# Kernel optimization log

Hardware: AMD Instinct MI355X
Metric: run time of the kernel (lower is better)

The kernel has to match this reference:

```python
import jax, jax.numpy as jnp
import numpy as np

B, SQ, SKV, DIN, DOUT = 8, 2048, 2048, 512, 512

def setup_inputs() -> dict:
    key = jax.random.key(0)
    ks = jax.random.split(key, 8)
    s = 1.0 / np.sqrt(DIN)
    return {
        "query": jax.random.normal(ks[0], (B, SQ, DIN), jnp.float32),
        "key": jax.random.normal(ks[1], (B, SKV, DIN), jnp.float32),
        "value": jax.random.normal(ks[2], (B, SKV, DIN), jnp.float32),
        "offset": jax.random.normal(ks[3], (B, SQ, DIN), jnp.float32),
        "Wq": jax.random.normal(ks[4], (DIN, DOUT), jnp.float32) * s,
        "Wk": jax.random.normal(ks[5], (DIN, DOUT), jnp.float32) * s,
        "Wv": jax.random.normal(ks[6], (DIN, DOUT), jnp.float32) * s,
        "Woff": jax.random.normal(ks[7], (DIN, SKV), jnp.float32) * s,
    }

def reference(query, key, value, offset, Wq, Wk, Wv, Woff):
    # q/k/v projections (nn.Linear, no bias)
    q = jnp.einsum("bqi,io->bqo", query, Wq)   # [B,SQ,DOUT]
    k = jnp.einsum("bki,io->bko", key, Wk)     # [B,SKV,DOUT]
    v = jnp.einsum("bki,io->bko", value, Wv)   # [B,SKV,DOUT]
    scale = 1.0 / jnp.sqrt(jnp.asarray(q.shape[-1], jnp.float32))
    scores = jnp.einsum("bqd,bkd->bqk", q, k) * scale  # [B,SQ,SKV]
    attn = jax.nn.softmax(scores, axis=-1)
    # offset bias is added AFTER softmax (no renormalization), per original
    attn = attn + jnp.einsum("bqi,ik->bqk", offset, Woff)
    return jnp.einsum("bqk,bkd->bqd", attn, v)  # [B,SQ,DOUT]
```

## Files before the change

### kernel.cpp

```cpp
#include <hip/hip_runtime.h>
#include <hip/hip_bf16.h>
#include <stdint.h>

typedef __bf16 bf16;
typedef bf16 bf16x4_t __attribute__((ext_vector_type(4)));
typedef bf16 bf16x8_t __attribute__((ext_vector_type(8)));
typedef float floatx4_t __attribute__((ext_vector_type(4)));

#define NB 8
#define SQ 2048
#define SKV 2048
#define DIN 512
#define DOUT 512

__device__ __forceinline__ void load_lds16(const bf16* g, bf16* l) {
    __builtin_amdgcn_global_load_lds(
        (const __attribute__((address_space(1))) unsigned int*)g,
        (__attribute__((address_space(3))) unsigned int*)l, 16, 0, 0);
}

struct CastArgs {
    const float* src[6];
    bf16* dst[6];
    int n4[6];
};
__global__ void cast_many(CastArgs a) {
    int z = blockIdx.z;
    int i = blockIdx.x * blockDim.x + threadIdx.x;
    if (i >= a.n4[z]) return;
    if (!a.src[z]) {
        bf16x4_t zo = { (bf16)0.f, (bf16)0.f, (bf16)0.f, (bf16)0.f };
        ((bf16x4_t*)a.dst[z])[i] = zo;
        return;
    }
    float4 f = ((const float4*)a.src[z])[i];
    bf16x4_t o = { (bf16)f.x, (bf16)f.y, (bf16)f.z, (bf16)f.w };
    ((bf16x4_t*)a.dst[z])[i] = o;
}

struct TWArgs { const float* src[3]; bf16* dst[3]; float scl[3]; };
__global__ void transpose_w(TWArgs a) {
    __shared__ float t[32][33];
    const float* src = a.src[blockIdx.z];
    bf16* dst = a.dst[blockIdx.z];
    const float s = a.scl[blockIdx.z];
    int tx = threadIdx.x, ty = threadIdx.y;
    int x0 = blockIdx.x * 32, y0 = blockIdx.y * 32;
#pragma unroll
    for (int j = 0; j < 4; ++j)
        t[ty + 8 * j][tx] = src[(y0 + ty + 8 * j) * DIN + x0 + tx];
    __syncthreads();
#pragma unroll
    for (int j = 0; j < 4; ++j)
        dst[(x0 + ty + 8 * j) * DIN + y0 + tx] = (bf16)(t[tx][ty + 8 * j] * s);
}

__device__ __forceinline__ void gemm_mainloop(
    floatx4_t (&acc)[4][4], const bf16* __restrict__ Ap, const bf16* __restrict__ Bp,
    int lda, int ldb, int K, bf16* As, bf16* Bs, int wave, int lane)
{
    const int wm = (wave & 1) * 64, wn = (wave >> 1) * 64;
    const int lm = lane & 15, quad = lane >> 4;
    const int srow = lane >> 2, scol = (lane & 3) * 8;
    for (int k0 = 0; k0 < K; k0 += 64) {
        __syncthreads();
#pragma unroll
        for (int p = 0; p < 2; ++p) {
#pragma unroll
            for (int t = 0; t < 2; ++t) {
                const int r0 = (wave * 2 + t) * 16;
                load_lds16(Ap + (long long)(r0 + srow) * lda + (k0 + p * 32 + scol),
                           &As[p * 4096 + r0 * 32]);
                load_lds16(Bp + (long long)(r0 + srow) * ldb + (k0 + p * 32 + scol),
                           &Bs[p * 4096 + r0 * 32]);
            }
        }
        __syncthreads();
#pragma unroll
        for (int p = 0; p < 2; ++p) {
            bf16x8_t af[4], bfr[4];
#pragma unroll
            for (int i = 0; i < 4; ++i)
                af[i] = *(const bf16x8_t*)&As[p * 4096 + (wm + i * 16 + lm) * 32 + quad * 8];
#pragma unroll
            for (int i = 0; i < 4; ++i)
                bfr[i] = *(const bf16x8_t*)&Bs[p * 4096 + (wn + i * 16 + lm) * 32 + quad * 8];
#pragma unroll
            for (int i = 0; i < 4; ++i)
#pragma unroll
                for (int j = 0; j < 4; ++j)
                    acc[i][j] = __builtin_amdgcn_mfma_f32_16x16x32_bf16(af[i], bfr[j], acc[i][j], 0, 0, 0);
        }
    }
}

__global__ __launch_bounds__(256) void proj_gemm(
    const bf16* __restrict__ QKin, const bf16* __restrict__ WqkT, bf16* __restrict__ QKout,
    const bf16* __restrict__ valueb, const bf16* __restrict__ WvT, bf16* __restrict__ VT)
{
    __shared__ bf16 As[2 * 128 * 32];
    __shared__ bf16 Bs[2 * 128 * 32];
    const int tid = threadIdx.x;
    const int wave = tid >> 6, lane = tid & 63;
    const int wm = (wave & 1) * 64, wn = (wave >> 1) * 64;
    const int lm = lane & 15, quad = lane >> 4;
    const int id = blockIdx.x;

    floatx4_t acc[4][4];
#pragma unroll
    for (int i = 0; i < 4; ++i)
#pragma unroll
        for (int j = 0; j < 4; ++j) acc[i][j] = 0.0f;

    if (id < 1024) {
        const int xcd = id & 7, t = id >> 3, m = t & 3;
        const int gg = xcd + 8 * (t >> 2);
        const int y = gg & 127, z = gg >> 7;
        const bf16* Ap = QKin + (long long)z * (NB * SQ * DIN) + (long long)y * 128 * DIN;
        const bf16* Bp = WqkT + (long long)z * (DIN * DOUT) + (long long)m * 128 * DIN;
        gemm_mainloop(acc, Ap, Bp, DIN, DIN, DIN, As, Bs, wave, lane);
        bf16* C = QKout + (long long)z * (NB * SQ * DOUT);
#pragma unroll
        for (int i = 0; i < 4; ++i)
#pragma unroll
            for (int j = 0; j < 4; ++j) {
                const long long row0 = (long long)y * 128 + wm + i * 16 + quad * 4;
                const int col = m * 128 + wn + j * 16 + lm;
#pragma unroll
                for (int r = 0; r < 4; ++r)
                    C[(row0 + r) * DOUT + col] = (bf16)acc[i][j][r];
            }
    } else {
        const int id2 = id - 1024;
        const int z = id2 & 7, r2 = id2 >> 3;
        const int ym = r2 & 3, xn = r2 >> 2;
        const bf16* Ap = WvT + (long long)ym * 128 * DIN;
        const bf16* Bp = valueb + (long long)z * (SKV * DIN) + (long long)xn * 128 * DIN;
        gemm_mainloop(acc, Ap, Bp, DIN, DIN, DIN, As, Bs, wave, lane);
        bf16* C = VT + (long long)z * (DOUT * SKV);
#pragma unroll
        for (int i = 0; i < 4; ++i)
#pragma unroll
            for (int j = 0; j < 4; ++j) {
                const long long row0 = (long long)ym * 128 + wm + i * 16 + quad * 4;
                const int col = xn * 128 + wn + j * 16 + lm;
#pragma unroll
                for (int r = 0; r < 4; ++r)
                    C[(row0 + r) * SKV + col] = (bf16)acc[i][j][r];
            }
    }
}

__global__ __launch_bounds__(256) void g_gemm(
    const bf16* __restrict__ VT, const bf16* __restrict__ Woffb, bf16* __restrict__ G)
{
    __shared__ bf16 As[2 * 128 * 32];
    __shared__ bf16 Bs[2 * 128 * 32];
    const int tid = threadIdx.x;
    const int wave = tid >> 6, lane = tid & 63;
    const int id = blockIdx.x;
    const int z = id & 7, x = (id >> 3) & 3, y = (id >> 3) >> 2;

    floatx4_t acc[4][4];
#pragma unroll
    for (int i = 0; i < 4; ++i)
#pragma unroll
        for (int j = 0; j < 4; ++j) acc[i][j] = 0.0f;

    const bf16* Ap = VT + (long long)z * (DOUT * SKV) + (long long)y * 128 * SKV;
    const bf16* Bp = Woffb + (long long)x * 128 * SKV;
    gemm_mainloop(acc, Ap, Bp, SKV, SKV, SKV, As, Bs, wave, lane);

    const int wm = (wave & 1) * 64, wn = (wave >> 1) * 64;
    const int lm = lane & 15, quad = lane >> 4;
    bf16* C = G + (long long)z * (DOUT * DIN);
#pragma unroll
    for (int i = 0; i < 4; ++i)
#pragma unroll
        for (int j = 0; j < 4; ++j) {
            const long long row0 = (long long)y * 128 + wm + i * 16 + quad * 4;
            const int col = x * 128 + wn + j * 16 + lm;
#pragma unroll
            for (int r = 0; r < 4; ++r)
                C[(row0 + r) * DIN + col] = (bf16)acc[i][j][r];
        }
}

__global__ __launch_bounds__(256) void s_gemm_exp(
    const bf16* __restrict__ Qb, const bf16* __restrict__ Kb,
    bf16* __restrict__ expS, float* __restrict__ l)
{
    __shared__ bf16 As[2 * 128 * 32];
    __shared__ bf16 Bs[2 * 128 * 32];
    const int tid = threadIdx.x;
    const int wave = tid >> 6, lane = tid & 63;
    const int id = blockIdx.x;
    const int z = id & 7, x = (id >> 3) & 15, y = (id >> 3) >> 4;

    floatx4_t acc[4][4];
#pragma unroll
    for (int i = 0; i < 4; ++i)
#pragma unroll
        for (int j = 0; j < 4; ++j) acc[i][j] = 0.0f;

    const bf16* Ap = Qb + ((long long)z * SQ + (long long)y * 128) * DOUT;
    const bf16* Bp = Kb + ((long long)z * SKV + (long long)x * 128) * DOUT;
    gemm_mainloop(acc, Ap, Bp, DOUT, DOUT, DOUT, As, Bs, wave, lane);

    const int wm = (wave & 1) * 64, wn = (wave >> 1) * 64;
    const int lm = lane & 15, quad = lane >> 4;
    bf16* C = expS + (long long)z * SQ * SKV;
    const long long grow0 = (long long)z * SQ + (long long)y * 128;
#pragma unroll
    for (int i = 0; i < 4; ++i) {
        float rs[4] = {0.f, 0.f, 0.f, 0.f};
#pragma unroll
        for (int j = 0; j < 4; ++j) {
            const long long row0 = (long long)y * 128 + wm + i * 16 + quad * 4;
            const int col = x * 128 + wn + j * 16 + lm;
#pragma unroll
            for (int r = 0; r < 4; ++r) {
                float e = __expf(acc[i][j][r]);
                rs[r] += e;
                C[(row0 + r) * SKV + col] = (bf16)e;
            }
        }
#pragma unroll
        for (int r = 0; r < 4; ++r) {
            float v = rs[r];
            v += __shfl_xor(v, 1, 64);
            v += __shfl_xor(v, 2, 64);
            v += __shfl_xor(v, 4, 64);
            v += __shfl_xor(v, 8, 64);
            if (lm == 0)
                atomicAdd(&l[grow0 + wm + i * 16 + quad * 4 + r], v);
        }
    }
}

__global__ __launch_bounds__(256) void out_gemm(
    const bf16* __restrict__ expS, const bf16* __restrict__ VT,
    const bf16* __restrict__ offb, const bf16* __restrict__ G,
    const float* __restrict__ l, float* __restrict__ out)
{
    __shared__ bf16 As[2 * 128 * 32];
    __shared__ bf16 Bs[2 * 128 * 32];
    const int tid = threadIdx.x;
    const int wave = tid >> 6, lane = tid & 63;
    const int id = blockIdx.x;
    const int z = id & 7, x = (id >> 3) & 3, y = (id >> 3) >> 2;

    floatx4_t acc[4][4];
#pragma unroll
    for (int i = 0; i < 4; ++i)
#pragma unroll
        for (int j = 0; j < 4; ++j) acc[i][j] = 0.0f;

    {
        const bf16* Ap = expS + (long long)z * SQ * SKV + (long long)y * 128 * SKV;
        const bf16* Bp = VT + (long long)z * DOUT * SKV + (long long)x * 128 * SKV;
        gemm_mainloop(acc, Ap, Bp, SKV, SKV, SKV, As, Bs, wave, lane);
    }

    const int wm = (wave & 1) * 64, wn = (wave >> 1) * 64;
    const int lm = lane & 15, quad = lane >> 4;
    const long long grow0 = (long long)z * SQ + (long long)y * 128;

#pragma unroll
    for (int i = 0; i < 4; ++i)
#pragma unroll
        for (int r = 0; r < 4; ++r) {
            const float inv = 1.0f / l[grow0 + wm + i * 16 + quad * 4 + r];
#pragma unroll
            for (int j = 0; j < 4; ++j) acc[i][j][r] *= inv;
        }

    {
        const bf16* Ap = offb + (grow0) * DIN;
        const bf16* Bp = G + (long long)z * DOUT * DIN + (long long)x * 128 * DIN;
        gemm_mainloop(acc, Ap, Bp, DIN, DIN, DIN, As, Bs, wave, lane);
    }

#pragma unroll
    for (int i = 0; i < 4; ++i)
#pragma unroll
        for (int j = 0; j < 4; ++j) {
            const long long row0 = grow0 + wm + i * 16 + quad * 4;
            const int col = x * 128 + wn + j * 16 + lm;
#pragma unroll
            for (int r = 0; r < 4; ++r)
                out[(row0 + r) * DOUT + col] = acc[i][j][r];
        }
}

extern "C" void kernel_launch(void* const* d_in, const int* in_sizes, int n_in,
                              void* d_out, int out_size, void* d_ws, size_t ws_size,
                              hipStream_t stream) {
    const float* query = (const float*)d_in[0];
    const float* key_ = (const float*)d_in[1];
    const float* value = (const float*)d_in[2];
    const float* offset = (const float*)d_in[3];
    const float* Wq = (const float*)d_in[4];
    const float* Wk = (const float*)d_in[5];
    const float* Wv = (const float*)d_in[6];
    const float* Woff = (const float*)d_in[7];
    float* out = (float*)d_out;

    char* ws = (char*)d_ws;
    const long long NE = (long long)NB * SQ * DIN;

    const long long MB = 1048576;
    bf16* queryb  = (bf16*)(ws + 0 * MB);
    bf16* keyb    = (bf16*)(ws + 16 * MB);
    bf16* valueb  = (bf16*)(ws + 32 * MB);
    bf16* offsetb = (bf16*)(ws + 48 * MB);
    bf16* Qb      = (bf16*)(ws + 64 * MB);
    bf16* Kb      = (bf16*)(ws + 80 * MB);
    bf16* VT      = (bf16*)(ws + 96 * MB);
    bf16* G       = (bf16*)(ws + 112 * MB);
    bf16* WqT     = (bf16*)(ws + 116 * MB);
    bf16* WkT     = (bf16*)(ws + 116 * MB + 524288);
    bf16* WvT     = (bf16*)(ws + 116 * MB + 1048576);
    bf16* Woffb   = (bf16*)(ws + 116 * MB + 1572864);
    float* lbuf   = (float*)(ws + 120 * MB);
    bf16* expS    = (bf16*)(ws + 121 * MB);

    CastArgs ca;
    ca.src[0] = query;  ca.dst[0] = queryb;  ca.n4[0] = (int)(NE / 4);
    ca.src[1] = key_;   ca.dst[1] = keyb;    ca.n4[1] = (int)(NE / 4);
    ca.src[2] = value;  ca.dst[2] = valueb;  ca.n4[2] = (int)(NE / 4);
    ca.src[3] = offset; ca.dst[3] = offsetb; ca.n4[3] = (int)(NE / 4);
    ca.src[4] = Woff;   ca.dst[4] = Woffb;   ca.n4[4] = (DIN * SKV) / 4;
    ca.src[5] = nullptr; ca.dst[5] = (bf16*)lbuf; ca.n4[5] = (NB * SQ * 4) / 8;
    cast_many<<<dim3(8192, 1, 6), 256, 0, stream>>>(ca);

    TWArgs tw;
    tw.src[0] = Wq; tw.src[1] = Wk; tw.src[2] = Wv;
    tw.dst[0] = WqT; tw.dst[1] = WkT; tw.dst[2] = WvT;
    tw.scl[0] = 0.04419417382415922f; tw.scl[1] = 1.0f; tw.scl[2] = 1.0f;
    transpose_w<<<dim3(16, 16, 3), dim3(32, 8), 0, stream>>>(tw);

    proj_gemm<<<dim3(1536), 256, 0, stream>>>(queryb, WqT, Qb, valueb, WvT, VT);

    g_gemm<<<dim3(128), 256, 0, stream>>>(VT, Woffb, G);

    s_gemm_exp<<<dim3(2048), 256, 0, stream>>>(Qb, Kb, expS, lbuf);

    out_gemm<<<dim3(512), 256, 0, stream>>>(expS, VT, offsetb, G, lbuf, out);
}
```

Baseline: 374.8 us.

## Move Q/K projection, score and PV GEMMs to FP8 with swizzled LDS layout

Query/key inputs, Wq/Wk, Q, K, exp(scores) and V^T are now stored as FP8 in an XOR-swizzled layout. The QK projection, score GEMM and P·V GEMM run on a new FP8 MFMA mainloop with a 128-wide K step, which halves memory traffic and raises MFMA throughput on those paths. The softmax scale moves into the exponent, and exp values are prescaled by 1/16 so they fit FP8 range, then undone by a factor of 16 at normalisation. The G GEMM is split in two halves along K into fp32 partials, which are summed into bf16 by extra blocks added to the score kernel, doubling that GEMM's parallelism. The cost is FP8 accuracy risk and an extra FP8 copy of V written alongside the bf16 one.

```diff
diff --git a/kernel.cpp b/kernel.cpp
--- a/kernel.cpp
+++ b/kernel.cpp
@@ -3,6 +3,7 @@
 #include <stdint.h>
 
 typedef __bf16 bf16;
+typedef unsigned char u8;
 typedef bf16 bf16x4_t __attribute__((ext_vector_type(4)));
 typedef bf16 bf16x8_t __attribute__((ext_vector_type(8)));
 typedef float floatx4_t __attribute__((ext_vector_type(4)));
@@ -13,46 +14,79 @@
 #define DIN 512
 #define DOUT 512
 
-__device__ __forceinline__ void load_lds16(const bf16* g, bf16* l) {
+#define SCORE_SCALE 0.0027621358640099513f
+#define P_STORE_SCALE 0.0625f
+#define P_UNDO_SCALE 16.0f
+
+__device__ __forceinline__ void load_lds16(const void* g, void* l) {
     __builtin_amdgcn_global_load_lds(
         (const __attribute__((address_space(1))) unsigned int*)g,
         (__attribute__((address_space(3))) unsigned int*)l, 16, 0, 0);
 }
 
+__device__ __forceinline__ u8 to_fp8(float f) {
+    int v = __builtin_amdgcn_cvt_pk_fp8_f32(f, 0.f, 0, false);
+    return (u8)(v & 0xff);
+}
+__device__ __forceinline__ unsigned int pack_fp8x4(float a, float b, float c, float d) {
+    int lo = __builtin_amdgcn_cvt_pk_fp8_f32(a, b, 0, false);
+    int all = __builtin_amdgcn_cvt_pk_fp8_f32(c, d, lo, true);
+    return (unsigned int)all;
+}
+
+__device__ __forceinline__ int swz_off(int row, int col) {
+    return (col & ~127) | ((((col >> 4) & 7) ^ (row & 7)) << 4) | (col & 15);
+}
+
 struct CastArgs {
     const float* src[6];
-    bf16* dst[6];
+    void* dst[6];
     int n4[6];
+    int mode[6];
 };
 __global__ void cast_many(CastArgs a) {
     int z = blockIdx.z;
     int i = blockIdx.x * blockDim.x + threadIdx.x;
     if (i >= a.n4[z]) return;
-    if (!a.src[z]) {
-        bf16x4_t zo = { (bf16)0.f, (bf16)0.f, (bf16)0.f, (bf16)0.f };
-        ((bf16x4_t*)a.dst[z])[i] = zo;
+    if (a.mode[z] == 2) {
+        ((float4*)a.dst[z])[i] = make_float4(0.f, 0.f, 0.f, 0.f);
         return;
     }
     float4 f = ((const float4*)a.src[z])[i];
-    bf16x4_t o = { (bf16)f.x, (bf16)f.y, (bf16)f.z, (bf16)f.w };
-    ((bf16x4_t*)a.dst[z])[i] = o;
-}
-
-struct TWArgs { const float* src[3]; bf16* dst[3]; float scl[3]; };
+    if (a.mode[z] == 1) {
+        int row = i >> 7;
+        int k0 = (i & 127) * 4;
+        u8* d = (u8*)a.dst[z];
+        *(unsigned int*)&d[row * 512 + swz_off(row, k0)] = pack_fp8x4(f.x, f.y, f.z, f.w);
+    } else {
+        bf16x4_t o = { (bf16)f.x, (bf16)f.y, (bf16)f.z, (bf16)f.w };
+        ((bf16x4_t*)a.dst[z])[i] = o;
+    }
+}
+
+struct TWArgs { const float* src[3]; void* dst[3]; };
 __global__ void transpose_w(TWArgs a) {
     __shared__ float t[32][33];
     const float* src = a.src[blockIdx.z];
-    bf16* dst = a.dst[blockIdx.z];
-    const float s = a.scl[blockIdx.z];
     int tx = threadIdx.x, ty = threadIdx.y;
     int x0 = blockIdx.x * 32, y0 = blockIdx.y * 32;
 #pragma unroll
     for (int j = 0; j < 4; ++j)
         t[ty + 8 * j][tx] = src[(y0 + ty + 8 * j) * DIN + x0 + tx];
     __syncthreads();
-#pragma unroll
-    for (int j = 0; j < 4; ++j)
-        dst[(x0 + ty + 8 * j) * DIN + y0 + tx] = (bf16)(t[tx][ty + 8 * j] * s);
+    if (blockIdx.z <= 1) {
+        u8* d8 = (u8*)a.dst[blockIdx.z];
+#pragma unroll
+        for (int j = 0; j < 4; ++j) {
+            int row = x0 + ty + 8 * j, col = y0 + tx;
+            d8[row * 512 + swz_off(row, col)] = to_fp8(t[tx][ty + 8 * j] * 4.0f);
+        }
+    } else {
+        bf16* db = (bf16*)a.dst[2];
+#pragma unroll
+        for (int j = 0; j < 4; ++j)
+            db[(x0 + ty + 8 * j) * DIN + y0 + tx] = (bf16)t[tx][ty + 8 * j];
+    }
 }
 
 __device__ __forceinline__ void gemm_mainloop(
@@ -94,12 +128,53 @@
     }
 }
 
+__device__ __forceinline__ void gemm_mainloop_fp8(
+    floatx4_t (&acc)[4][4], const u8* __restrict__ Ap, const u8* __restrict__ Bp,
+    int lda, int ldb, int K, u8* As, u8* Bs, int wave, int lane)
+{
+    const int wm = (wave & 1) * 64, wn = (wave >> 1) * 64;
+    const int lm = lane & 15, quad = lane >> 4;
+    const int srow = lane >> 3, scol = (lane & 7) * 16;
+    const int x7 = lm & 7;
+    const int inner = (quad & 1) * 8;
+    const int gh = quad >> 1;
+    for (int k0 = 0; k0 < K; k0 += 128) {
+        __syncthreads();
+#pragma unroll
+        for (int t = 0; t < 4; ++t) {
+            const int r0 = (wave * 4 + t) * 8;
+            load_lds16(Ap + (long long)(r0 + srow) * lda + k0 + scol, &As[r0 * 128]);
+            load_lds16(Bp + (long long)(r0 + srow) * ldb + k0 + scol, &Bs[r0 * 128]);
+        }
+        __syncthreads();
+#pragma unroll
+        for (int p = 0; p < 4; ++p) {
+            const int gL = p * 2 + gh;
+            const int koff = ((gL ^ x7) << 4) + inner;
+            long long a[4], b[4];
+#pragma unroll
+            for (int i = 0; i < 4; ++i)
+                a[i] = *(const long long*)&As[(wm + i * 16 + lm) * 128 + koff];
+#pragma unroll
+            for (int i = 0; i < 4; ++i)
+                b[i] = *(const long long*)&Bs[(wn + i * 16 + lm) * 128 + koff];
+#pragma unroll
+            for (int i = 0; i < 4; ++i)
+#pragma unroll
+                for (int j = 0; j < 4; ++j)
+                    acc[i][j] = __builtin_amdgcn_mfma_f32_16x16x32_fp8_fp8(a[i], b[j], acc[i][j], 0, 0, 0);
+        }
+    }
+}
+
 __global__ __launch_bounds__(256) void proj_gemm(
-    const bf16* __restrict__ QKin, const bf16* __restrict__ WqkT, bf16* __restrict__ QKout,
-    const bf16* __restrict__ valueb, const bf16* __restrict__ WvT, bf16* __restrict__ VT)
-{
-    __shared__ bf16 As[2 * 128 * 32];
-    __shared__ bf16 Bs[2 * 128 * 32];
+    const u8* __restrict__ query8, const u8* __restrict__ key8,
+    const u8* __restrict__ WqT8, const u8* __restrict__ WkT8,
+    u8* __restrict__ Qb8, u8* __restrict__ Kb8,
+    const bf16* __restrict__ valueb, const bf16* __restrict__ WvT,
+    bf16* __restrict__ VT, u8* __restrict__ VT8)
+{
+    __shared__ __align__(16) u8 smem[32768];
     const int tid = threadIdx.x;
     const int wave = tid >> 6, lane = tid & 63;
     const int wm = (wave & 1) * 64, wn = (wave >> 1) * 64;
@@ -116,19 +191,19 @@
         const int xcd = id & 7, t = id >> 3, m = t & 3;
         const int gg = xcd + 8 * (t >> 2);
         const int y = gg & 127, z = gg >> 7;
-        const bf16* Ap = QKin + (long long)z * (NB * SQ * DIN) + (long long)y * 128 * DIN;
-        const bf16* Bp = WqkT + (long long)z * (DIN * DOUT) + (long long)m * 128 * DIN;
-        gemm_mainloop(acc, Ap, Bp, DIN, DIN, DIN, As, Bs, wave, lane);
-        bf16* C = QKout + (long long)z * (NB * SQ * DOUT);
+        const u8* Ap = (z ? key8 : query8) + (long long)y * 128 * DIN;
+        const u8* Bp = (z ? WkT8 : WqT8) + (long long)m * 128 * DIN;
+        gemm_mainloop_fp8(acc, Ap, Bp, DIN, DIN, DIN, smem, smem + 16384, wave, lane);
+        u8* C = z ? Kb8 : Qb8;
 #pragma unroll
         for (int i = 0; i < 4; ++i)
 #pragma unroll
             for (int j = 0; j < 4; ++j) {
-                const long long row0 = (long long)y * 128 + wm + i * 16 + quad * 4;
+                const int row0 = y * 128 + wm + i * 16 + quad * 4;
                 const int col = m * 128 + wn + j * 16 + lm;
 #pragma unroll
                 for (int r = 0; r < 4; ++r)
-                    C[(row0 + r) * DOUT + col] = (bf16)acc[i][j][r];
+                    C[(long long)(row0 + r) * DOUT + swz_off(row0 + r, col)] = to_fp8(acc[i][j][r]);
             }
     } else {
         const int id2 = id - 1024;
@@ -136,30 +211,34 @@
         const int ym = r2 & 3, xn = r2 >> 2;
         const bf16* Ap = WvT + (long long)ym * 128 * DIN;
         const bf16* Bp = valueb + (long long)z * (SKV * DIN) + (long long)xn * 128 * DIN;
-        gemm_mainloop(acc, Ap, Bp, DIN, DIN, DIN, As, Bs, wave, lane);
+        gemm_mainloop(acc, Ap, Bp, DIN, DIN, DIN, (bf16*)smem, (bf16*)(smem + 16384), wave, lane);
         bf16* C = VT + (long long)z * (DOUT * SKV);
+        u8* C8 = VT8 + (long long)z * (DOUT * SKV);
 #pragma unroll
         for (int i = 0; i < 4; ++i)
 #pragma unroll
             for (int j = 0; j < 4; ++j) {
-                const long long row0 = (long long)ym * 128 + wm + i * 16 + quad * 4;
+                const int row0 = ym * 128 + wm + i * 16 + quad * 4;
                 const int col = xn * 128 + wn + j * 16 + lm;
 #pragma unroll
-                for (int r = 0; r < 4; ++r)
-                    C[(row0 + r) * SKV + col] = (bf16)acc[i][j][r];
+                for (int r = 0; r < 4; ++r) {
+                    float v = acc[i][j][r];
+                    C[(long long)(row0 + r) * SKV + col] = (bf16)v;
+                    C8[(long long)(row0 + r) * SKV + swz_off(row0 + r, col)] = to_fp8(v);
+                }
             }
     }
 }
 
 __global__ __launch_bounds__(256) void g_gemm(
-    const bf16* __restrict__ VT, const bf16* __restrict__ Woffb, bf16* __restrict__ G)
-{
-    __shared__ bf16 As[2 * 128 * 32];
-    __shared__ bf16 Bs[2 * 128 * 32];
+    const bf16* __restrict__ VT, const bf16* __restrict__ Woffb,
+    float* __restrict__ G32a, float* __restrict__ G32b)
+{
+    __shared__ __align__(16) u8 smem[32768];
     const int tid = threadIdx.x;
     const int wave = tid >> 6, lane = tid & 63;
     const int id = blockIdx.x;
-    const int z = id & 7, x = (id >> 3) & 3, y = (id >> 3) >> 2;
+    const int z = id & 7, h = (id >> 3) & 1, x = (id >> 4) & 3, y = (id >> 6) & 3;
 
     floatx4_t acc[4][4];
 #pragma unroll
@@ -167,34 +246,50 @@
 #pragma unroll
         for (int j = 0; j < 4; ++j) acc[i][j] = 0.0f;
 
-    const bf16* Ap = VT + (long long)z * (DOUT * SKV) + (long long)y * 128 * SKV;
-    const bf16* Bp = Woffb + (long long)x * 128 * SKV;
-    gemm_mainloop(acc, Ap, Bp, SKV, SKV, SKV, As, Bs, wave, lane);
-
-    const int wm = (wave & 1) * 64, wn = (wave >> 1) * 64;
-    const int lm = lane & 15, quad = lane >> 4;
-    bf16* C = G + (long long)z * (DOUT * DIN);
+    const bf16* Ap = VT + (long long)z * (DOUT * SKV) + (long long)y * 128 * SKV + h * 1024;
+    const bf16* Bp = Woffb + (long long)x * 128 * SKV + h * 1024;
+    gemm_mainloop(acc, Ap, Bp, SKV, SKV, 1024, (bf16*)smem, (bf16*)(smem + 16384), wave, lane);
+
+    const int wm = (wave & 1) * 64, wn = (wave >> 1) * 64;
+    const int lm = lane & 15, quad = lane >> 4;
+    float* C = (h ? G32b : G32a) + (long long)z * (DOUT * DIN);
 #pragma unroll
     for (int i = 0; i < 4; ++i)
 #pragma unroll
         for (int j = 0; j < 4; ++j) {
-            const long long row0 = (long long)y * 128 + wm + i * 16 + quad * 4;
+            const int row0 = y * 128 + wm + i * 16 + quad * 4;
             const int col = x * 128 + wn + j * 16 + lm;
 #pragma unroll
             for (int r = 0; r < 4; ++r)
-                C[(row0 + r) * DIN + col] = (bf16)acc[i][j][r];
+                C[(long long)(row0 + r) * DIN + col] = acc[i][j][r];
         }
 }
 
 __global__ __launch_bounds__(256) void s_gemm_exp(
-    const bf16* __restrict__ Qb, const bf16* __restrict__ Kb,
-    bf16* __restrict__ expS, float* __restrict__ l)
-{
-    __shared__ bf16 As[2 * 128 * 32];
-    __shared__ bf16 Bs[2 * 128 * 32];
+    const u8* __restrict__ Qb8, const u8* __restrict__ Kb8,
+    u8* __restrict__ expS8, float* __restrict__ l,
+    const float* __restrict__ G32a, const float* __restrict__ G32b,
+    bf16* __restrict__ Gb)
+{
+    __shared__ __align__(16) u8 smem[32768];
     const int tid = threadIdx.x;
+    const int id = blockIdx.x;
+    if (id >= 2048) {
+        const int base = (id - 2048) * 256 + tid;
+        const float4* A4 = (const float4*)G32a;
+        const float4* B4 = (const float4*)G32b;
+        bf16x4_t* O4 = (bf16x4_t*)Gb;
+#pragma unroll 4
+        for (int t = 0; t < 32; ++t) {
+            const int idx = base + t * 16384;
+            float4 a = A4[idx], b = B4[idx];
+            bf16x4_t o = { (bf16)(a.x + b.x), (bf16)(a.y + b.y),
+                           (bf16)(a.z + b.z), (bf16)(a.w + b.w) };
+            O4[idx] = o;
+        }
+        return;
+    }
     const int wave = tid >> 6, lane = tid & 63;
-    const int id = blockIdx.x;
     const int z = id & 7, x = (id >> 3) & 15, y = (id >> 3) >> 4;
 
     floatx4_t acc[4][4];
@@ -203,26 +298,26 @@
 #pragma unroll
         for (int j = 0; j < 4; ++j) acc[i][j] = 0.0f;
 
-    const bf16* Ap = Qb + ((long long)z * SQ + (long long)y * 128) * DOUT;
-    const bf16* Bp = Kb + ((long long)z * SKV + (long long)x * 128) * DOUT;
-    gemm_mainloop(acc, Ap, Bp, DOUT, DOUT, DOUT, As, Bs, wave, lane);
-
-    const int wm = (wave & 1) * 64, wn = (wave >> 1) * 64;
-    const int lm = lane & 15, quad = lane >> 4;
-    bf16* C = expS + (long long)z * SQ * SKV;
+    const u8* Ap = Qb8 + ((long long)z * SQ + (long long)y * 128) * DOUT;
+    const u8* Bp = Kb8 + ((long long)z * SKV + (long long)x * 128) * DOUT;
+    gemm_mainloop_fp8(acc, Ap, Bp, DOUT, DOUT, DOUT, smem, smem + 16384, wave, lane);
+
+    const int wm = (wave & 1) * 64, wn = (wave >> 1) * 64;
+    const int lm = lane & 15, quad = lane >> 4;
+    u8* C = expS8 + (long long)z * SQ * SKV;
     const long long grow0 = (long long)z * SQ + (long long)y * 128;
 #pragma unroll
     for (int i = 0; i < 4; ++i) {
         float rs[4] = {0.f, 0.f, 0.f, 0.f};
 #pragma unroll
         for (int j = 0; j < 4; ++j) {
-            const long long row0 = (long long)y * 128 + wm + i * 16 + quad * 4;
+            const int row0 = y * 128 + wm + i * 16 + quad * 4;
             const int col = x * 128 + wn + j * 16 + lm;
 #pragma unroll
             for (int r = 0; r < 4; ++r) {
-                float e = __expf(acc[i][j][r]);
+                float e = __expf(acc[i][j][r] * SCORE_SCALE);
                 rs[r] += e;
-                C[(row0 + r) * SKV + col] = (bf16)e;
+                C[(long long)(row0 + r) * SKV + swz_off(row0 + r, col)] = to_fp8(e * P_STORE_SCALE);
             }
         }
 #pragma unroll
@@ -239,12 +334,11 @@
 }
 
 __global__ __launch_bounds__(256) void out_gemm(
-    const bf16* __restrict__ expS, const bf16* __restrict__ VT,
-    const bf16* __restrict__ offb, const bf16* __restrict__ G,
+    const u8* __restrict__ expS8, const u8* __restrict__ VT8,
+    const bf16* __restrict__ offb, const bf16* __restrict__ Gb,
     const float* __restrict__ l, float* __restrict__ out)
 {
-    __shared__ bf16 As[2 * 128 * 32];
-    __shared__ bf16 Bs[2 * 128 * 32];
+    __shared__ __align__(16) u8 smem[32768];
     const int tid = threadIdx.x;
     const int wave = tid >> 6, lane = tid & 63;
     const int id = blockIdx.x;
@@ -257,9 +351,9 @@
         for (int j = 0; j < 4; ++j) acc[i][j] = 0.0f;
 
     {
-        const bf16* Ap = expS + (long long)z * SQ * SKV + (long long)y * 128 * SKV;
-        const bf16* Bp = VT + (long long)z * DOUT * SKV + (long long)x * 128 * SKV;
-        gemm_mainloop(acc, Ap, Bp, SKV, SKV, SKV, As, Bs, wave, lane);
+        const u8* Ap = expS8 + (long long)z * SQ * SKV + (long long)y * 128 * SKV;
+        const u8* Bp = VT8 + (long long)z * DOUT * SKV + (long long)x * 128 * SKV;
+        gemm_mainloop_fp8(acc, Ap, Bp, SKV, SKV, SKV, smem, smem + 16384, wave, lane);
     }
 
     const int wm = (wave & 1) * 64, wn = (wave >> 1) * 64;
@@ -270,15 +364,15 @@
     for (int i = 0; i < 4; ++i)
 #pragma unroll
         for (int r = 0; r < 4; ++r) {
-            const float inv = 1.0f / l[grow0 + wm + i * 16 + quad * 4 + r];
+            const float inv = P_UNDO_SCALE / l[grow0 + wm + i * 16 + quad * 4 + r];
 #pragma unroll
             for (int j = 0; j < 4; ++j) acc[i][j][r] *= inv;
         }
 
     {
-        const bf16* Ap = offb + (grow0) * DIN;
-        const bf16* Bp = G + (long long)z * DOUT * DIN + (long long)x * 128 * DIN;
-        gemm_mainloop(acc, Ap, Bp, DIN, DIN, DIN, As, Bs, wave, lane);
+        const bf16* Ap = offb + grow0 * DIN;
+        const bf16* Bp = Gb + (long long)z * DOUT * DIN + (long long)x * 128 * DIN;
+        gemm_mainloop(acc, Ap, Bp, DIN, DIN, DIN, (bf16*)smem, (bf16*)(smem + 16384), wave, lane);
     }
 
 #pragma unroll
@@ -308,43 +402,46 @@
 
     char* ws = (char*)d_ws;
     const long long NE = (long long)NB * SQ * DIN;
-
     const long long MB = 1048576;
-    bf16* queryb  = (bf16*)(ws + 0 * MB);
-    bf16* keyb    = (bf16*)(ws + 16 * MB);
-    bf16* valueb  = (bf16*)(ws + 32 * MB);
-    bf16* offsetb = (bf16*)(ws + 48 * MB);
-    bf16* Qb      = (bf16*)(ws + 64 * MB);
-    bf16* Kb      = (bf16*)(ws + 80 * MB);
-    bf16* VT      = (bf16*)(ws + 96 * MB);
-    bf16* G       = (bf16*)(ws + 112 * MB);
-    bf16* WqT     = (bf16*)(ws + 116 * MB);
-    bf16* WkT     = (bf16*)(ws + 116 * MB + 524288);
-    bf16* WvT     = (bf16*)(ws + 116 * MB + 1048576);
-    bf16* Woffb   = (bf16*)(ws + 116 * MB + 1572864);
-    float* lbuf   = (float*)(ws + 120 * MB);
-    bf16* expS    = (bf16*)(ws + 121 * MB);
+
+    u8* query8   = (u8*)(ws + 0 * MB);
+    u8* key8     = (u8*)(ws + 8 * MB);
+    bf16* valueb = (bf16*)(ws + 16 * MB);
+    bf16* offsetb= (bf16*)(ws + 32 * MB);
+    u8* Qb8      = (u8*)(ws + 48 * MB);
+    u8* Kb8      = (u8*)(ws + 56 * MB);
+    bf16* VT     = (bf16*)(ws + 64 * MB);
+    u8* VT8      = (u8*)(ws + 80 * MB);
+    float* G32a  = (float*)(ws + 88 * MB);
+    float* G32b  = (float*)(ws + 96 * MB);
+    bf16* Gb     = (bf16*)(ws + 104 * MB);
+    u8* WqT8     = (u8*)(ws + 108 * MB);
+    u8* WkT8     = (u8*)(ws + 108 * MB + 262144);
+    bf16* WvT    = (bf16*)(ws + 108 * MB + 524288);
+    bf16* Woffb  = (bf16*)(ws + 109 * MB);
+    float* lbuf  = (float*)(ws + 111 * MB);
+    u8* expS8    = (u8*)(ws + 112 * MB);
 
     CastArgs ca;
-    ca.src[0] = query;  ca.dst[0] = queryb;  ca.n4[0] = (int)(NE / 4);
-    ca.src[1] = key_;   ca.dst[1] = keyb;    ca.n4[1] = (int)(NE / 4);
-    ca.src[2] = value;  ca.dst[2] = valueb;  ca.n4[2] = (int)(NE / 4);
-    ca.src[3] = offset; ca.dst[3] = offsetb; ca.n4[3] = (int)(NE / 4);
-    ca.src[4] = Woff;   ca.dst[4] = Woffb;   ca.n4[4] = (DIN * SKV) / 4;
-    ca.src[5] = nullptr; ca.dst[5] = (bf16*)lbuf; ca.n4[5] = (NB * SQ * 4) / 8;
+    ca.src[0] = query;  ca.dst[0] = query8;  ca.n4[0] = (int)(NE / 4); ca.mode[0] = 1;
+    ca.src[1] = key_;   ca.dst[1] = key8;    ca.n4[1] = (int)(NE / 4); ca.mode[1] = 1;
+    ca.src[2] = value;  ca.dst[2] = valueb;  ca.n4[2] = (int)(NE / 4); ca.mode[2] = 0;
+    ca.src[3] = offset; ca.dst[3] = offsetb; ca.n4[3] = (int)(NE / 4); ca.mode[3] = 0;
+    ca.src[4] = Woff;   ca.dst[4] = Woffb;   ca.n4[4] = (DIN * SKV) / 4; ca.mode[4] = 0;
+    ca.src[5] = nullptr; ca.dst[5] = lbuf;   ca.n4[5] = (NB * SQ) / 4; ca.mode[5] = 2;
     cast_many<<<dim3(8192, 1, 6), 256, 0, stream>>>(ca);
 
     TWArgs tw;
     tw.src[0] = Wq; tw.src[1] = Wk; tw.src[2] = Wv;
-    tw.dst[0] = WqT; tw.dst[1] = WkT; tw.dst[2] = WvT;
-    tw.scl[0] = 0.04419417382415922f; tw.scl[1] = 1.0f; tw.scl[2] = 1.0f;
+    tw.dst[0] = WqT8; tw.dst[1] = WkT8; tw.dst[2] = WvT;
     transpose_w<<<dim3(16, 16, 3), dim3(32, 8), 0, stream>>>(tw);
 
-    proj_gemm<<<dim3(1536), 256, 0, stream>>>(queryb, WqT, Qb, valueb, WvT, VT);
-
-    g_gemm<<<dim3(128), 256, 0, stream>>>(VT, Woffb, G);
-
-    s_gemm_exp<<<dim3(2048), 256, 0, stream>>>(Qb, Kb, expS, lbuf);
-
-    out_gemm<<<dim3(512), 256, 0, stream>>>(expS, VT, offsetb, G, lbuf, out);
-}
+    proj_gemm<<<dim3(1536), 256, 0, stream>>>(query8, key8, WqT8, WkT8, Qb8, Kb8,
+                                              valueb, WvT, VT, VT8);
+
+    g_gemm<<<dim3(256), 256, 0, stream>>>(VT, Woffb, G32a, G32b);
+
+    s_gemm_exp<<<dim3(2112), 256, 0, stream>>>(Qb8, Kb8, expS8, lbuf, G32a, G32b, Gb);
+
+    out_gemm<<<dim3(512), 256, 0, stream>>>(expS8, VT8, offsetb, Gb, lbuf, out);
+}
```

Result: faster. 333.3 us (-11.1%).
